# Optimization experiments

Hardware: AMD Instinct MI355X
Metric: run time of the kernel (lower is better)

Reference implementation:

```python
import jax, jax.numpy as jnp
import numpy as np

N, E, G = 50000, 800000, 128
IN_DIM, HID, HEADS, OUT_DIM = 256, 64, 4, 10
HC = HID * HEADS  # 256
NEG_SLOPE = 0.2


def _gat_layer(x, src, dst, W, att_src, att_dst, bias):
    # x: [N, F_in]; W: [F_in, H*C]; att_*: [H, C]; bias: [H*C]
    n = x.shape[0]
    h = (x @ W).reshape(n, HEADS, HID)                      # [N,H,C]
    a_src = jnp.einsum('nhc,hc->nh', h, att_src)            # [N,H]
    a_dst = jnp.einsum('nhc,hc->nh', h, att_dst)            # [N,H]
    e = a_src[src] + a_dst[dst]                             # [E,H]
    e = jax.nn.leaky_relu(e, NEG_SLOPE)
    # segment softmax over incoming edges of each dst node
    m = jax.ops.segment_max(e, dst, num_segments=n)         # [N,H]
    ex = jnp.exp(e - m[dst])
    denom = jax.ops.segment_sum(ex, dst, num_segments=n)    # [N,H]
    alpha = ex / (denom[dst] + 1e-16)                       # [E,H]
    msg = h[src] * alpha[:, :, None]                        # [E,H,C]
    out = jax.ops.segment_sum(msg, dst, num_segments=n)     # [N,H,C]
    return out.reshape(n, HC) + bias


def setup_inputs() -> dict:
    key = jax.random.key(0)
    ks = jax.random.split(key, 16)
    x = jax.random.normal(ks[0], (N, IN_DIM), dtype=jnp.float32)
    edge_index = jax.random.randint(ks[1], (2, E), 0, N, dtype=jnp.int64)
    edge_weight = jax.random.uniform(ks[2], (E,), dtype=jnp.float32)
    batch = jnp.sort(jax.random.randint(ks[3], (N,), 0, G, dtype=jnp.int64))
    s = 0.05
    W1 = jax.random.normal(ks[4], (IN_DIM, HC), dtype=jnp.float32) * s
    att_src1 = jax.random.normal(ks[5], (HEADS, HID), dtype=jnp.float32) * s
    att_dst1 = jax.random.normal(ks[6], (HEADS, HID), dtype=jnp.float32) * s
    b1 = jnp.zeros((HC,), dtype=jnp.float32)
    W2 = jax.random.normal(ks[7], (HC, HC), dtype=jnp.float32) * s
    att_src2 = jax.random.normal(ks[8], (HEADS, HID), dtype=jnp.float32) * s
    att_dst2 = jax.random.normal(ks[9], (HEADS, HID), dtype=jnp.float32) * s
    b2 = jnp.zeros((HC,), dtype=jnp.float32)
    Wf = jax.random.normal(ks[10], (HC, OUT_DIM), dtype=jnp.float32) * s
    bf = jnp.zeros((OUT_DIM,), dtype=jnp.float32)
    return dict(x=x, edge_index=edge_index, edge_weight=edge_weight, batch=batch,
                W1=W1, att_src1=att_src1, att_dst1=att_dst1, b1=b1,
                W2=W2, att_src2=att_src2, att_dst2=att_dst2, b2=b2,
                Wf=Wf, bf=bf)


def reference(x, edge_index, edge_weight, batch,
              W1, att_src1, att_dst1, b1,
              W2, att_src2, att_dst2, b2,
              Wf, bf):
    n = x.shape[0]
    # add self loops (add_self_loops=True in GATConv)
    loop = jnp.arange(n, dtype=edge_index.dtype)
    ei = jnp.concatenate([edge_index, jnp.stack([loop, loop])], axis=1)
    src, dst = ei[0], ei[1]
    h = jax.nn.relu(_gat_layer(x, src, dst, W1, att_src1, att_dst1, b1))
    h = jax.nn.relu(_gat_layer(h, src, dst, W2, att_src2, att_dst2, b2))
    # global mean pool per graph
    counts = jax.ops.segment_sum(jnp.ones((n,), dtype=h.dtype), batch, num_segments=G)
    pooled = jax.ops.segment_sum(h, batch, num_segments=G) / jnp.maximum(counts, 1.0)[:, None]
    out = pooled @ Wf + bf
    return out, pooled
```

## Files before the change

kernel.cpp:

```cpp
#include <hip/hip_runtime.h>
#include <math.h>

#define HEADS 4
#define HID 64
#define HC 256
#define NEG_SLOPE 0.2f
#define GG 128

typedef __attribute__((ext_vector_type(8))) short short8;
typedef __attribute__((ext_vector_type(4))) float floatx4;
typedef unsigned short ush;

__device__ __forceinline__ ush f2bf(float f) {
  unsigned u = __float_as_uint(f);
  unsigned r = (u + 0x7FFFu + ((u >> 16) & 1u)) >> 16;
  return (ush)r;
}
__device__ __forceinline__ float bf2f(ush h) {
  return __uint_as_float(((unsigned)h) << 16);
}

__global__ void fill_counts_kernel(int* counts, int n) {
  int i = blockIdx.x * 256 + threadIdx.x;
  if (i < n) counts[i] = 1;
}

__global__ void hist_kernel(const int* __restrict__ ei, int* counts, int E) {
  int e = blockIdx.x * 256 + threadIdx.x;
  if (e < E) atomicAdd(&counts[ei[E + e]], 1);
}

__global__ __launch_bounds__(256) void scan_pass1(const int* __restrict__ counts,
                                                  int* __restrict__ bsums, int n) {
  int t = threadIdx.x;
  int i0 = blockIdx.x * 1024 + t * 4;
  int s = 0;
  if (i0 + 3 < n) {
    int4 v = *(const int4*)&counts[i0];
    s = v.x + v.y + v.z + v.w;
  } else {
#pragma unroll
    for (int k = 0; k < 4; ++k)
      if (i0 + k < n) s += counts[i0 + k];
  }
#pragma unroll
  for (int o = 1; o < 64; o <<= 1) s += __shfl_xor(s, o, 64);
  __shared__ int ws[4];
  if ((t & 63) == 0) ws[t >> 6] = s;
  __syncthreads();
  if (t == 0) bsums[blockIdx.x] = ws[0] + ws[1] + ws[2] + ws[3];
}

__global__ __launch_bounds__(256) void scan_pass2(int* __restrict__ bsums,
                                                  int* __restrict__ row_ptr, int nb, int n) {
  __shared__ int sh[256];
  int t = threadIdx.x;
  int v = (t < nb) ? bsums[t] : 0;
  sh[t] = v;
  __syncthreads();
  for (int off = 1; off < 256; off <<= 1) {
    int u = (t >= off) ? sh[t - off] : 0;
    __syncthreads();
    sh[t] += u;
    __syncthreads();
  }
  if (t < nb) bsums[t] = sh[t] - v;
  if (t == 255) row_ptr[n] = sh[255];
}

__global__ __launch_bounds__(256) void scan_pass3(const int* __restrict__ counts,
                                                  const int* __restrict__ bsums,
                                                  int* __restrict__ row_ptr,
                                                  int* __restrict__ cursor, int n) {
  int t = threadIdx.x;
  int i0 = blockIdx.x * 1024 + t * 4;
  int c0 = 0, c1 = 0, c2 = 0, c3 = 0;
  bool full = (i0 + 3 < n);
  if (full) {
    int4 v = *(const int4*)&counts[i0];
    c0 = v.x; c1 = v.y; c2 = v.z; c3 = v.w;
  } else {
    if (i0 + 0 < n) c0 = counts[i0 + 0];
    if (i0 + 1 < n) c1 = counts[i0 + 1];
    if (i0 + 2 < n) c2 = counts[i0 + 2];
    if (i0 + 3 < n) c3 = counts[i0 + 3];
  }
  int ts = c0 + c1 + c2 + c3;
  __shared__ int sh[256];
  sh[t] = ts;
  __syncthreads();
  for (int off = 1; off < 256; off <<= 1) {
    int u = (t >= off) ? sh[t - off] : 0;
    __syncthreads();
    sh[t] += u;
    __syncthreads();
  }
  int run = bsums[blockIdx.x] + sh[t] - ts;
  int r0 = run, r1 = run + c0, r2 = r1 + c1, r3 = r2 + c2;
  if (full) {
    *(int4*)&row_ptr[i0] = make_int4(r0, r1, r2, r3);
    *(int4*)&cursor[i0] = make_int4(r0, r1, r2, r3);
  } else {
    if (i0 + 0 < n) { row_ptr[i0 + 0] = r0; cursor[i0 + 0] = r0; }
    if (i0 + 1 < n) { row_ptr[i0 + 1] = r1; cursor[i0 + 1] = r1; }
    if (i0 + 2 < n) { row_ptr[i0 + 2] = r2; cursor[i0 + 2] = r2; }
    if (i0 + 3 < n) { row_ptr[i0 + 3] = r3; cursor[i0 + 3] = r3; }
  }
}

__global__ void scatter_kernel(const int* __restrict__ ei, int* cursor, int* srcs, int E, int n) {
  int i = blockIdx.x * 256 + threadIdx.x;
  if (i >= E + n) return;
  int s, d;
  if (i < E) { s = ei[i]; d = ei[E + i]; }
  else       { s = i - E; d = s; }
  int pos = atomicAdd(&cursor[d], 1);
  srcs[pos] = s;
}

__global__ __launch_bounds__(256) void splitA_kernel(const float* __restrict__ A,
                                                     ush* __restrict__ Ah,
                                                     ush* __restrict__ Al, int total) {
  int i0 = (blockIdx.x * 256 + threadIdx.x) * 4;
  if (i0 + 3 < total) {
    float4 v = *(const float4*)&A[i0];
    ushort4 h = make_ushort4(f2bf(v.x), f2bf(v.y), f2bf(v.z), f2bf(v.w));
    ushort4 l = make_ushort4(f2bf(v.x - bf2f(h.x)), f2bf(v.y - bf2f(h.y)),
                             f2bf(v.z - bf2f(h.z)), f2bf(v.w - bf2f(h.w)));
    *(ushort4*)&Ah[i0] = h;
    *(ushort4*)&Al[i0] = l;
  } else {
    for (int k = 0; k < 4 && i0 + k < total; ++k) {
      float v = A[i0 + k];
      ush h = f2bf(v);
      Ah[i0 + k] = h;
      Al[i0 + k] = f2bf(v - bf2f(h));
    }
  }
}

__global__ void convertB_kernel(const float* __restrict__ B, ush* __restrict__ Bth,
                                ush* __restrict__ Btl) {
  int k = blockIdx.x, n = threadIdx.x;
  float v = B[k * HC + n];
  ush h = f2bf(v);
  ush l = f2bf(v - bf2f(h));
  Bth[n * HC + k] = h;
  Btl[n * HC + k] = l;
}

#define LDA 40
__global__ __launch_bounds__(256) void gemm_kernel(
    const ush* __restrict__ Ah, const ush* __restrict__ Al,
    const ush* __restrict__ Bth, const ush* __restrict__ Btl,
    const float* __restrict__ att_src, const float* __restrict__ att_dst,
    ush* __restrict__ Cb, float* __restrict__ asrc_o, float* __restrict__ adst_o, int M) {
  __shared__ ush sAh[128 * LDA];
  __shared__ ush sAl[128 * LDA];
  __shared__ ush sBh[128 * LDA];
  __shared__ ush sBl[128 * LDA];

  int t = threadIdx.x;
  int lane = t & 63, wave = t >> 6;
  int wm = wave >> 1, wn = wave & 1;
  int q = lane >> 4, mrow = lane & 15;
  int r0 = blockIdx.y * 128;
  int c0 = blockIdx.x * 128;

  int row0 = t >> 2, seg0 = t & 3;
  int row1 = (t + 256) >> 2, seg1 = (t + 256) & 3;
  bool v0 = (r0 + row0) < M, v1 = (r0 + row1) < M;
  const int4 zero4 = make_int4(0, 0, 0, 0);

  floatx4 acc[4][4];
#pragma unroll
  for (int i = 0; i < 4; ++i)
#pragma unroll
    for (int j = 0; j < 4; ++j) acc[i][j] = (floatx4)(0.0f);

  for (int k0 = 0; k0 < HC; k0 += 32) {
    __syncthreads();
    {
      size_t g0 = (size_t)(r0 + row0) * HC + k0 + seg0 * 8;
      size_t g1 = (size_t)(r0 + row1) * HC + k0 + seg1 * 8;
      *(int4*)&sAh[row0 * LDA + seg0 * 8] = v0 ? *(const int4*)&Ah[g0] : zero4;
      *(int4*)&sAh[row1 * LDA + seg1 * 8] = v1 ? *(const int4*)&Ah[g1] : zero4;
      *(int4*)&sAl[row0 * LDA + seg0 * 8] = v0 ? *(const int4*)&Al[g0] : zero4;
      *(int4*)&sAl[row1 * LDA + seg1 * 8] = v1 ? *(const int4*)&Al[g1] : zero4;
      size_t b0 = (size_t)(c0 + row0) * HC + k0 + seg0 * 8;
      size_t b1 = (size_t)(c0 + row1) * HC + k0 + seg1 * 8;
      *(int4*)&sBh[row0 * LDA + seg0 * 8] = *(const int4*)&Bth[b0];
      *(int4*)&sBh[row1 * LDA + seg1 * 8] = *(const int4*)&Bth[b1];
      *(int4*)&sBl[row0 * LDA + seg0 * 8] = *(const int4*)&Btl[b0];
      *(int4*)&sBl[row1 * LDA + seg1 * 8] = *(const int4*)&Btl[b1];
    }
    __syncthreads();

    short8 ah[4], al[4], bh[4], bl[4];
#pragma unroll
    for (int i = 0; i < 4; ++i) {
      int ar = (wm * 64 + i * 16 + mrow) * LDA + q * 8;
      int br = (wn * 64 + i * 16 + mrow) * LDA + q * 8;
      ah[i] = *(short8*)&sAh[ar];
      al[i] = *(short8*)&sAl[ar];
      bh[i] = *(short8*)&sBh[br];
      bl[i] = *(short8*)&sBl[br];
    }
#pragma unroll
    for (int i = 0; i < 4; ++i)
#pragma unroll
      for (int j = 0; j < 4; ++j) {
        acc[i][j] = __builtin_amdgcn_mfma_f32_16x16x32_bf16(ah[i], bh[j], acc[i][j], 0, 0, 0);
        acc[i][j] = __builtin_amdgcn_mfma_f32_16x16x32_bf16(ah[i], bl[j], acc[i][j], 0, 0, 0);
        acc[i][j] = __builtin_amdgcn_mfma_f32_16x16x32_bf16(al[i], bh[j], acc[i][j], 0, 0, 0);
      }
  }

  int hd = (c0 >> 6) + wn;
  float aS[4], aD[4];
#pragma unroll
  for (int j = 0; j < 4; ++j) {
    aS[j] = att_src[hd * 64 + j * 16 + mrow];
    aD[j] = att_dst[hd * 64 + j * 16 + mrow];
  }
#pragma unroll
  for (int i = 0; i < 4; ++i) {
#pragma unroll
    for (int r = 0; r < 4; ++r) {
      float ps = acc[i][0][r] * aS[0] + acc[i][1][r] * aS[1] +
                 acc[i][2][r] * aS[2] + acc[i][3][r] * aS[3];
      float pd = acc[i][0][r] * aD[0] + acc[i][1][r] * aD[1] +
                 acc[i][2][r] * aD[2] + acc[i][3][r] * aD[3];
#pragma unroll
      for (int o = 1; o < 16; o <<= 1) {
        ps += __shfl_xor(ps, o, 64);
        pd += __shfl_xor(pd, o, 64);
      }
      int grow = r0 + wm * 64 + i * 16 + q * 4 + r;
      if (mrow == 0 && grow < M) {
        asrc_o[grow * HEADS + hd] = ps;
        adst_o[grow * HEADS + hd] = pd;
      }
    }
  }

#pragma unroll
  for (int i = 0; i < 4; ++i) {
#pragma unroll
    for (int j = 0; j < 4; ++j) {
      int col = c0 + wn * 64 + j * 16 + mrow;
#pragma unroll
      for (int r = 0; r < 4; ++r) {
        int grow = r0 + wm * 64 + i * 16 + q * 4 + r;
        if (grow < M) Cb[(size_t)grow * HC + col] = f2bf(acc[i][j][r]);
      }
    }
  }
}

__device__ __forceinline__ float lrelu(float x) { return x > 0.f ? x : NEG_SLOPE * x; }

__global__ __launch_bounds__(256) void aggregate_kernel(
    const ush* __restrict__ hbf, const float* __restrict__ asrc,
    const float* __restrict__ adst, const int* __restrict__ row_ptr,
    const int* __restrict__ srcs, const float* __restrict__ bias,
    float* __restrict__ outf, ush* __restrict__ outh, ush* __restrict__ outl, int N) {
  __shared__ float s_alpha[4][64 * 4];
  __shared__ int s_src[4][64];

  int wave = threadIdx.x >> 6;
  int lane = threadIdx.x & 63;
  int node = blockIdx.x * 4 + wave;
  if (node >= N) return;

  int begin = row_ptr[node];
  int end = row_ptr[node + 1];
  int deg = end - begin;
  int nb = deg < 64 ? deg : 64;

  const float4* asrc4 = (const float4*)asrc;
  float4 ad = ((const float4*)adst)[node];

  const float NEGINF = -3.402823466e38f;
  int s0 = 0;
  float4 e0 = make_float4(NEGINF, NEGINF, NEGINF, NEGINF);
  if (lane < nb) {
    s0 = srcs[begin + lane];
    float4 a = asrc4[s0];
    e0.x = lrelu(a.x + ad.x);
    e0.y = lrelu(a.y + ad.y);
    e0.z = lrelu(a.z + ad.z);
    e0.w = lrelu(a.w + ad.w);
  }
  float m0 = e0.x, m1 = e0.y, m2 = e0.z, m3 = e0.w;
  for (int base = 64; base < deg; base += 64) {
    int idx = base + lane;
    if (idx < deg) {
      int s = srcs[begin + idx];
      float4 a = asrc4[s];
      m0 = fmaxf(m0, lrelu(a.x + ad.x));
      m1 = fmaxf(m1, lrelu(a.y + ad.y));
      m2 = fmaxf(m2, lrelu(a.z + ad.z));
      m3 = fmaxf(m3, lrelu(a.w + ad.w));
    }
  }
#pragma unroll
  for (int o = 1; o < 64; o <<= 1) {
    m0 = fmaxf(m0, __shfl_xor(m0, o, 64));
    m1 = fmaxf(m1, __shfl_xor(m1, o, 64));
    m2 = fmaxf(m2, __shfl_xor(m2, o, 64));
    m3 = fmaxf(m3, __shfl_xor(m3, o, 64));
  }
  float ex0 = (lane < nb) ? __expf(e0.x - m0) : 0.f;
  float ex1 = (lane < nb) ? __expf(e0.y - m1) : 0.f;
  float ex2 = (lane < nb) ? __expf(e0.z - m2) : 0.f;
  float ex3 = (lane < nb) ? __expf(e0.w - m3) : 0.f;
  float d0 = ex0, d1 = ex1, d2 = ex2, d3 = ex3;
  for (int base = 64; base < deg; base += 64) {
    int idx = base + lane;
    if (idx < deg) {
      int s = srcs[begin + idx];
      float4 a = asrc4[s];
      d0 += __expf(lrelu(a.x + ad.x) - m0);
      d1 += __expf(lrelu(a.y + ad.y) - m1);
      d2 += __expf(lrelu(a.z + ad.z) - m2);
      d3 += __expf(lrelu(a.w + ad.w) - m3);
    }
  }
#pragma unroll
  for (int o = 1; o < 64; o <<= 1) {
    d0 += __shfl_xor(d0, o, 64);
    d1 += __shfl_xor(d1, o, 64);
    d2 += __shfl_xor(d2, o, 64);
    d3 += __shfl_xor(d3, o, 64);
  }
  float r0 = 1.0f / (d0 + 1e-16f);
  float r1 = 1.0f / (d1 + 1e-16f);
  float r2 = 1.0f / (d2 + 1e-16f);
  float r3 = 1.0f / (d3 + 1e-16f);

  *(float4*)&s_alpha[wave][lane * 4] = make_float4(ex0 * r0, ex1 * r1, ex2 * r2, ex3 * r3);
  s_src[wave][lane] = s0;

  int head = lane >> 4;
  float mh = (head == 0) ? m0 : (head == 1) ? m1 : (head == 2) ? m2 : m3;
  float rdh = (head == 0) ? r0 : (head == 1) ? r1 : (head == 2) ? r2 : r3;
  float adh = (head == 0) ? ad.x : (head == 1) ? ad.y : (head == 2) ? ad.z : ad.w;

  const ushort4* hb4 = (const ushort4*)hbf;
  float4 accA = make_float4(0.f, 0.f, 0.f, 0.f);
  float4 accB = accA, accC = accA, accD = accA;
  int i = 0;
  for (; i + 4 <= nb; i += 4) {
    int sa = s_src[wave][i];
    int sb = s_src[wave][i + 1];
    int sc = s_src[wave][i + 2];
    int sd = s_src[wave][i + 3];
    float aa = s_alpha[wave][i * 4 + head];
    float ab = s_alpha[wave][(i + 1) * 4 + head];
    float ac = s_alpha[wave][(i + 2) * 4 + head];
    float ad_ = s_alpha[wave][(i + 3) * 4 + head];
    ushort4 u0 = hb4[(size_t)sa * 64 + lane];
    ushort4 u1 = hb4[(size_t)sb * 64 + lane];
    ushort4 u2 = hb4[(size_t)sc * 64 + lane];
    ushort4 u3 = hb4[(size_t)sd * 64 + lane];
    accA.x += aa * bf2f(u0.x); accA.y += aa * bf2f(u0.y);
    accA.z += aa * bf2f(u0.z); accA.w += aa * bf2f(u0.w);
    accB.x += ab * bf2f(u1.x); accB.y += ab * bf2f(u1.y);
    accB.z += ab * bf2f(u1.z); accB.w += ab * bf2f(u1.w);
    accC.x += ac * bf2f(u2.x); accC.y += ac * bf2f(u2.y);
    accC.z += ac * bf2f(u2.z); accC.w += ac * bf2f(u2.w);
    accD.x += ad_ * bf2f(u3.x); accD.y += ad_ * bf2f(u3.y);
    accD.z += ad_ * bf2f(u3.z); accD.w += ad_ * bf2f(u3.w);
  }
  for (; i < nb; ++i) {
    int s = s_src[wave][i];
    float a = s_alpha[wave][i * 4 + head];
    ushort4 u = hb4[(size_t)s * 64 + lane];
    accA.x += a * bf2f(u.x); accA.y += a * bf2f(u.y);
    accA.z += a * bf2f(u.z); accA.w += a * bf2f(u.w);
  }
  for (int i2 = 64; i2 < deg; ++i2) {
    int s = srcs[begin + i2];
    float ash = asrc[s * HEADS + head];
    float a = __expf(lrelu(ash + adh) - mh) * rdh;
    ushort4 u = hb4[(size_t)s * 64 + lane];
    accA.x += a * bf2f(u.x); accA.y += a * bf2f(u.y);
    accA.z += a * bf2f(u.z); accA.w += a * bf2f(u.w);
  }

  float4 acc;
  acc.x = (accA.x + accB.x) + (accC.x + accD.x);
  acc.y = (accA.y + accB.y) + (accC.y + accD.y);
  acc.z = (accA.z + accB.z) + (accC.z + accD.z);
  acc.w = (accA.w + accB.w) + (accC.w + accD.w);
  float4 bv = ((const float4*)bias)[lane];
  float4 o;
  o.x = fmaxf(acc.x + bv.x, 0.f);
  o.y = fmaxf(acc.y + bv.y, 0.f);
  o.z = fmaxf(acc.z + bv.z, 0.f);
  o.w = fmaxf(acc.w + bv.w, 0.f);

  if (outf) {
    ((float4*)outf)[(size_t)node * 64 + lane] = o;
  } else {
    ushort4 h = make_ushort4(f2bf(o.x), f2bf(o.y), f2bf(o.z), f2bf(o.w));
    ushort4 l = make_ushort4(f2bf(o.x - bf2f(h.x)), f2bf(o.y - bf2f(h.y)),
                             f2bf(o.z - bf2f(h.z)), f2bf(o.w - bf2f(h.w)));
    ((ushort4*)outh)[(size_t)node * 64 + lane] = h;
    ((ushort4*)outl)[(size_t)node * 64 + lane] = l;
  }
}

__device__ __forceinline__ int lower_bound_i(const int* a, int n, int key) {
  int lo = 0, hi = n;
  while (lo < hi) {
    int mid = (lo + hi) >> 1;
    if (a[mid] < key) lo = mid + 1; else hi = mid;
  }
  return lo;
}

__global__ __launch_bounds__(256) void pool_kernel(const float* __restrict__ h2,
                                                   const int* __restrict__ batch,
                                                   float* __restrict__ pws,
                                                   int* __restrict__ cnts, int n) {
  int g = blockIdx.x, part = blockIdx.y;
  int wave = threadIdx.x >> 6, lane = threadIdx.x & 63;
  int lo = lower_bound_i(batch, n, g);
  int hi = lower_bound_i(batch, n, g + 1);
  const float4* h4 = (const float4*)h2;
  float4 acc = make_float4(0.f, 0.f, 0.f, 0.f);
  for (int i = lo + part * 4 + wave; i < hi; i += 16) {
    float4 v = h4[(size_t)i * 64 + lane];
    acc.x += v.x; acc.y += v.y; acc.z += v.z; acc.w += v.w;
  }
  __shared__ float4 red[4][64];
  red[wave][lane] = acc;
  __syncthreads();
  if (wave == 0) {
    float4 a0 = red[0][lane], a1 = red[1][lane], a2 = red[2][lane], a3 = red[3][lane];
    float4 o;
    o.x = (a0.x + a1.x) + (a2.x + a3.x);
    o.y = (a0.y + a1.y) + (a2.y + a3.y);
    o.z = (a0.z + a1.z) + (a2.z + a3.z);
    o.w = (a0.w + a1.w) + (a2.w + a3.w);
    ((float4*)pws)[(size_t)(g * 4 + part) * 64 + lane] = o;
  }
  if (part == 0 && threadIdx.x == 0) cnts[g] = hi - lo;
}

__global__ void final_kernel(const float* __restrict__ pws, const int* __restrict__ cnts,
                             const float* __restrict__ Wf, const float* __restrict__ bf,
                             float* __restrict__ pooled_out, float* __restrict__ out) {
  int g = blockIdx.x, t = threadIdx.x;
  float s = pws[(size_t)(g * 4 + 0) * 256 + t] + pws[(size_t)(g * 4 + 1) * 256 + t] +
            pws[(size_t)(g * 4 + 2) * 256 + t] + pws[(size_t)(g * 4 + 3) * 256 + t];
  float inv = 1.0f / fmaxf((float)cnts[g], 1.0f);
  float pv = s * inv;
  pooled_out[g * HC + t] = pv;
  __shared__ float p[HC];
  p[t] = pv;
  __syncthreads();
  if (t < 10) {
    float acc = bf[t];
    for (int c = 0; c < HC; ++c) acc += p[c] * Wf[c * 10 + t];
    out[g * 10 + t] = acc;
  }
}

extern "C" void kernel_launch(void* const* d_in, const int* in_sizes, int n_in,
                              void* d_out, int out_size, void* d_ws, size_t ws_size,
                              hipStream_t stream) {
  const float* x    = (const float*)d_in[0];
  const int*   ei   = (const int*)d_in[1];
  const int*   batch = (const int*)d_in[3];
  const float* W1   = (const float*)d_in[4];
  const float* as1  = (const float*)d_in[5];
  const float* ad1  = (const float*)d_in[6];
  const float* b1   = (const float*)d_in[7];
  const float* W2   = (const float*)d_in[8];
  const float* as2  = (const float*)d_in[9];
  const float* ad2  = (const float*)d_in[10];
  const float* b2   = (const float*)d_in[11];
  const float* Wf   = (const float*)d_in[12];
  const float* bf   = (const float*)d_in[13];
  float* out = (float*)d_out;

  const int N = in_sizes[0] / HC;
  const int E = in_sizes[1] / 2;

  char* base = (char*)d_ws;
  size_t off = 0;
  auto alloc = [&](size_t bytes) {
    char* p = base + off;
    off = (off + bytes + 255) & ~(size_t)255;
    return p;
  };
  ush* xh = (ush*)alloc((size_t)N * HC * 2);
  ush* xl = (ush*)alloc((size_t)N * HC * 2);
  float* bufB = (float*)xh;
  ush* hbf = (ush*)alloc((size_t)N * HC * 2);
  float* asrc = (float*)alloc((size_t)N * HEADS * 4);
  float* adst = (float*)alloc((size_t)N * HEADS * 4);
  int* counts = (int*)alloc((size_t)N * 4);
  int* row_ptr = (int*)alloc((size_t)(N + 1) * 4);
  int* cursor = (int*)alloc((size_t)N * 4);
  int* srcs = (int*)alloc((size_t)(E + N) * 4);
  int* bsums = (int*)alloc(((N + 1023) / 1024) * 4);
  ush* Bth = (ush*)alloc((size_t)HC * HC * 2);
  ush* Btl = (ush*)alloc((size_t)HC * HC * 2);
  float* pws = (float*)alloc((size_t)GG * 4 * HC * 4);
  int* cnts = (int*)alloc((size_t)GG * 4);

  int nb = (N + 1023) / 1024;

  fill_counts_kernel<<<(N + 255) / 256, 256, 0, stream>>>(counts, N);
  hist_kernel<<<(E + 255) / 256, 256, 0, stream>>>(ei, counts, E);
  scan_pass1<<<nb, 256, 0, stream>>>(counts, bsums, N);
  scan_pass2<<<1, 256, 0, stream>>>(bsums, row_ptr, nb, N);
  scan_pass3<<<nb, 256, 0, stream>>>(counts, bsums, row_ptr, cursor, N);
  scatter_kernel<<<(E + N + 255) / 256, 256, 0, stream>>>(ei, cursor, srcs, E, N);

  dim3 ggrid(2, (N + 127) / 128);
  int agg_blocks = (N + 3) / 4;

  splitA_kernel<<<(N * HC / 4 + 255) / 256, 256, 0, stream>>>(x, xh, xl, N * HC);

  convertB_kernel<<<HC, HC, 0, stream>>>(W1, Bth, Btl);
  gemm_kernel<<<ggrid, 256, 0, stream>>>(xh, xl, Bth, Btl, as1, ad1, hbf, asrc, adst, N);
  aggregate_kernel<<<agg_blocks, 256, 0, stream>>>(hbf, asrc, adst, row_ptr, srcs, b1,
                                                   nullptr, xh, xl, N);

  convertB_kernel<<<HC, HC, 0, stream>>>(W2, Bth, Btl);
  gemm_kernel<<<ggrid, 256, 0, stream>>>(xh, xl, Bth, Btl, as2, ad2, hbf, asrc, adst, N);
  aggregate_kernel<<<agg_blocks, 256, 0, stream>>>(hbf, asrc, adst, row_ptr, srcs, b2,
                                                   bufB, nullptr, nullptr, N);

  dim3 pgrid(GG, 4);
  pool_kernel<<<pgrid, 256, 0, stream>>>(bufB, batch, pws, cnts, N);
  final_kernel<<<GG, 256, 0, stream>>>(pws, cnts, Wf, bf, out + GG * 10, out);
}
```

Measured before the change: 482.3 us.

## Widen GEMM tile to full 256 columns, store layer-2 output as bf16, merge setup kernels

```diff
diff --git a/kernel.cpp b/kernel.cpp
--- a/kernel.cpp
+++ b/kernel.cpp
@@ -20,14 +20,11 @@
   return __uint_as_float(((unsigned)h) << 16);
 }
 
-__global__ void fill_counts_kernel(int* counts, int n) {
+__global__ void hist_kernel(const int* __restrict__ ei, int* counts, int E, int n) {
   int i = blockIdx.x * 256 + threadIdx.x;
-  if (i < n) counts[i] = 1;
-}
-
-__global__ void hist_kernel(const int* __restrict__ ei, int* counts, int E) {
-  int e = blockIdx.x * 256 + threadIdx.x;
-  if (e < E) atomicAdd(&counts[ei[E + e]], 1);
+  if (i >= E + n) return;
+  int d = (i < E) ? ei[E + i] : (i - E);
+  atomicAdd(&counts[d], 1);
 }
 
 __global__ __launch_bounds__(256) void scan_pass1(const int* __restrict__ counts,
@@ -139,14 +136,18 @@
   }
 }
 
-__global__ void convertB_kernel(const float* __restrict__ B, ush* __restrict__ Bth,
-                                ush* __restrict__ Btl) {
+__global__ void convertB_kernel(const float* __restrict__ W1, const float* __restrict__ W2,
+                                ush* __restrict__ Bth1, ush* __restrict__ Btl1,
+                                ush* __restrict__ Bth2, ush* __restrict__ Btl2) {
   int k = blockIdx.x, n = threadIdx.x;
+  const float* B = blockIdx.y ? W2 : W1;
+  ush* th = blockIdx.y ? Bth2 : Bth1;
+  ush* tl = blockIdx.y ? Btl2 : Btl1;
   float v = B[k * HC + n];
   ush h = f2bf(v);
   ush l = f2bf(v - bf2f(h));
-  Bth[n * HC + k] = h;
-  Btl[n * HC + k] = l;
+  th[n * HC + k] = h;
+  tl[n * HC + k] = l;
 }
 
 #define LDA 40
@@ -157,98 +158,102 @@
     ush* __restrict__ Cb, float* __restrict__ asrc_o, float* __restrict__ adst_o, int M) {
   __shared__ ush sAh[128 * LDA];
   __shared__ ush sAl[128 * LDA];
-  __shared__ ush sBh[128 * LDA];
-  __shared__ ush sBl[128 * LDA];
+  __shared__ ush sBh[256 * LDA];
+  __shared__ ush sBl[256 * LDA];
 
   int t = threadIdx.x;
   int lane = t & 63, wave = t >> 6;
   int wm = wave >> 1, wn = wave & 1;
   int q = lane >> 4, mrow = lane & 15;
-  int r0 = blockIdx.y * 128;
-  int c0 = blockIdx.x * 128;
-
-  int row0 = t >> 2, seg0 = t & 3;
-  int row1 = (t + 256) >> 2, seg1 = (t + 256) & 3;
-  bool v0 = (r0 + row0) < M, v1 = (r0 + row1) < M;
+  int r0 = blockIdx.x * 128;
   const int4 zero4 = make_int4(0, 0, 0, 0);
 
-  floatx4 acc[4][4];
+  floatx4 acc[4][8];
 #pragma unroll
   for (int i = 0; i < 4; ++i)
 #pragma unroll
-    for (int j = 0; j < 4; ++j) acc[i][j] = (floatx4)(0.0f);
+    for (int j = 0; j < 8; ++j) acc[i][j] = (floatx4)(0.0f);
+
+  int ar0 = t >> 2, as0 = t & 3;
+  int ar1 = (t + 256) >> 2, as1 = (t + 256) & 3;
+  bool av0 = (r0 + ar0) < M, av1 = (r0 + ar1) < M;
 
   for (int k0 = 0; k0 < HC; k0 += 32) {
     __syncthreads();
     {
-      size_t g0 = (size_t)(r0 + row0) * HC + k0 + seg0 * 8;
-      size_t g1 = (size_t)(r0 + row1) * HC + k0 + seg1 * 8;
-      *(int4*)&sAh[row0 * LDA + seg0 * 8] = v0 ? *(const int4*)&Ah[g0] : zero4;
-      *(int4*)&sAh[row1 * LDA + seg1 * 8] = v1 ? *(const int4*)&Ah[g1] : zero4;
-      *(int4*)&sAl[row0 * LDA + seg0 * 8] = v0 ? *(const int4*)&Al[g0] : zero4;
-      *(int4*)&sAl[row1 * LDA + seg1 * 8] = v1 ? *(const int4*)&Al[g1] : zero4;
-      size_t b0 = (size_t)(c0 + row0) * HC + k0 + seg0 * 8;
-      size_t b1 = (size_t)(c0 + row1) * HC + k0 + seg1 * 8;
-      *(int4*)&sBh[row0 * LDA + seg0 * 8] = *(const int4*)&Bth[b0];
-      *(int4*)&sBh[row1 * LDA + seg1 * 8] = *(const int4*)&Bth[b1];
-      *(int4*)&sBl[row0 * LDA + seg0 * 8] = *(const int4*)&Btl[b0];
-      *(int4*)&sBl[row1 * LDA + seg1 * 8] = *(const int4*)&Btl[b1];
+      size_t g0 = (size_t)(r0 + ar0) * HC + k0 + as0 * 8;
+      size_t g1 = (size_t)(r0 + ar1) * HC + k0 + as1 * 8;
+      *(int4*)&sAh[ar0 * LDA + as0 * 8] = av0 ? *(const int4*)&Ah[g0] : zero4;
+      *(int4*)&sAh[ar1 * LDA + as1 * 8] = av1 ? *(const int4*)&Ah[g1] : zero4;
+      *(int4*)&sAl[ar0 * LDA + as0 * 8] = av0 ? *(const int4*)&Al[g0] : zero4;
+      *(int4*)&sAl[ar1 * LDA + as1 * 8] = av1 ? *(const int4*)&Al[g1] : zero4;
+#pragma unroll
+      for (int tau = 0; tau < 1024; tau += 256) {
+        int br = (t + tau) >> 2, bs = (t + tau) & 3;
+        size_t gb = (size_t)br * HC + k0 + bs * 8;
+        *(int4*)&sBh[br * LDA + bs * 8] = *(const int4*)&Bth[gb];
+        *(int4*)&sBl[br * LDA + bs * 8] = *(const int4*)&Btl[gb];
+      }
     }
     __syncthreads();
 
-    short8 ah[4], al[4], bh[4], bl[4];
+    short8 ah[4], al[4];
 #pragma unroll
     for (int i = 0; i < 4; ++i) {
       int ar = (wm * 64 + i * 16 + mrow) * LDA + q * 8;
-      int br = (wn * 64 + i * 16 + mrow) * LDA + q * 8;
       ah[i] = *(short8*)&sAh[ar];
       al[i] = *(short8*)&sAl[ar];
-      bh[i] = *(short8*)&sBh[br];
-      bl[i] = *(short8*)&sBl[br];
-    }
-#pragma unroll
-    for (int i = 0; i < 4; ++i)
-#pragma unroll
-      for (int j = 0; j < 4; ++j) {
-        acc[i][j] = __builtin_amdgcn_mfma_f32_16x16x32_bf16(ah[i], bh[j], acc[i][j], 0, 0, 0);
-        acc[i][j] = __builtin_amdgcn_mfma_f32_16x16x32_bf16(ah[i], bl[j], acc[i][j], 0, 0, 0);
-        acc[i][j] = __builtin_amdgcn_mfma_f32_16x16x32_bf16(al[i], bh[j], acc[i][j], 0, 0, 0);
+    }
+#pragma unroll
+    for (int j = 0; j < 8; ++j) {
+      int br = (wn * 128 + j * 16 + mrow) * LDA + q * 8;
+      short8 bh = *(short8*)&sBh[br];
+      short8 bl = *(short8*)&sBl[br];
+#pragma unroll
+      for (int i = 0; i < 4; ++i) {
+        acc[i][j] = __builtin_amdgcn_mfma_f32_16x16x32_bf16(ah[i], bh, acc[i][j], 0, 0, 0);
+        acc[i][j] = __builtin_amdgcn_mfma_f32_16x16x32_bf16(ah[i], bl, acc[i][j], 0, 0, 0);
+        acc[i][j] = __builtin_amdgcn_mfma_f32_16x16x32_bf16(al[i], bh, acc[i][j], 0, 0, 0);
       }
-  }
-
-  int hd = (c0 >> 6) + wn;
-  float aS[4], aD[4];
-#pragma unroll
-  for (int j = 0; j < 4; ++j) {
-    aS[j] = att_src[hd * 64 + j * 16 + mrow];
-    aD[j] = att_dst[hd * 64 + j * 16 + mrow];
-  }
+    }
+  }
+
+#pragma unroll
+  for (int jh = 0; jh < 2; ++jh) {
+    int hd = wn * 2 + jh;
+    float aS[4], aD[4];
+#pragma unroll
+    for (int jj = 0; jj < 4; ++jj) {
+      aS[jj] = att_src[hd * 64 + jj * 16 + mrow];
+      aD[jj] = att_dst[hd * 64 + jj * 16 + mrow];
+    }
+#pragma unroll
+    for (int i = 0; i < 4; ++i) {
+#pragma unroll
+      for (int r = 0; r < 4; ++r) {
+        float ps = acc[i][jh * 4 + 0][r] * aS[0] + acc[i][jh * 4 + 1][r] * aS[1] +
+                   acc[i][jh * 4 + 2][r] * aS[2] + acc[i][jh * 4 + 3][r] * aS[3];
+        float pd = acc[i][jh * 4 + 0][r] * aD[0] + acc[i][jh * 4 + 1][r] * aD[1] +
+                   acc[i][jh * 4 + 2][r] * aD[2] + acc[i][jh * 4 + 3][r] * aD[3];
+#pragma unroll
+        for (int o = 1; o < 16; o <<= 1) {
+          ps += __shfl_xor(ps, o, 64);
+          pd += __shfl_xor(pd, o, 64);
+        }
+        int grow = r0 + wm * 64 + i * 16 + q * 4 + r;
+        if (mrow == 0 && grow < M) {
+          asrc_o[grow * HEADS + hd] = ps;
+          adst_o[grow * HEADS + hd] = pd;
+        }
+      }
+    }
+  }
+
 #pragma unroll
   for (int i = 0; i < 4; ++i) {
 #pragma unroll
-    for (int r = 0; r < 4; ++r) {
-      float ps = acc[i][0][r] * aS[0] + acc[i][1][r] * aS[1] +
-                 acc[i][2][r] * aS[2] + acc[i][3][r] * aS[3];
-      float pd = acc[i][0][r] * aD[0] + acc[i][1][r] * aD[1] +
-                 acc[i][2][r] * aD[2] + acc[i][3][r] * aD[3];
-#pragma unroll
-      for (int o = 1; o < 16; o <<= 1) {
-        ps += __shfl_xor(ps, o, 64);
-        pd += __shfl_xor(pd, o, 64);
-      }
-      int grow = r0 + wm * 64 + i * 16 + q * 4 + r;
-      if (mrow == 0 && grow < M) {
-        asrc_o[grow * HEADS + hd] = ps;
-        adst_o[grow * HEADS + hd] = pd;
-      }
-    }
-  }
-
-#pragma unroll
-  for (int i = 0; i < 4; ++i) {
-#pragma unroll
-    for (int j = 0; j < 4; ++j) {
-      int col = c0 + wn * 64 + j * 16 + mrow;
+    for (int j = 0; j < 8; ++j) {
+      int col = wn * 128 + j * 16 + mrow;
 #pragma unroll
       for (int r = 0; r < 4; ++r) {
         int grow = r0 + wm * 64 + i * 16 + q * 4 + r;
@@ -405,10 +410,12 @@
     ((float4*)outf)[(size_t)node * 64 + lane] = o;
   } else {
     ushort4 h = make_ushort4(f2bf(o.x), f2bf(o.y), f2bf(o.z), f2bf(o.w));
-    ushort4 l = make_ushort4(f2bf(o.x - bf2f(h.x)), f2bf(o.y - bf2f(h.y)),
-                             f2bf(o.z - bf2f(h.z)), f2bf(o.w - bf2f(h.w)));
     ((ushort4*)outh)[(size_t)node * 64 + lane] = h;
-    ((ushort4*)outl)[(size_t)node * 64 + lane] = l;
+    if (outl) {
+      ushort4 l = make_ushort4(f2bf(o.x - bf2f(h.x)), f2bf(o.y - bf2f(h.y)),
+                               f2bf(o.z - bf2f(h.z)), f2bf(o.w - bf2f(h.w)));
+      ((ushort4*)outl)[(size_t)node * 64 + lane] = l;
+    }
   }
 }
 
@@ -421,7 +428,7 @@
   return lo;
 }
 
-__global__ __launch_bounds__(256) void pool_kernel(const float* __restrict__ h2,
+__global__ __launch_bounds__(256) void pool_kernel(const ush* __restrict__ h2,
                                                    const int* __restrict__ batch,
                                                    float* __restrict__ pws,
                                                    int* __restrict__ cnts, int n) {
@@ -429,11 +436,12 @@
   int wave = threadIdx.x >> 6, lane = threadIdx.x & 63;
   int lo = lower_bound_i(batch, n, g);
   int hi = lower_bound_i(batch, n, g + 1);
-  const float4* h4 = (const float4*)h2;
+  const ushort4* h4 = (const ushort4*)h2;
   float4 acc = make_float4(0.f, 0.f, 0.f, 0.f);
   for (int i = lo + part * 4 + wave; i < hi; i += 16) {
-    float4 v = h4[(size_t)i * 64 + lane];
-    acc.x += v.x; acc.y += v.y; acc.z += v.z; acc.w += v.w;
+    ushort4 u = h4[(size_t)i * 64 + lane];
+    acc.x += bf2f(u.x); acc.y += bf2f(u.y);
+    acc.z += bf2f(u.z); acc.w += bf2f(u.w);
   }
   __shared__ float4 red[4][64];
   red[wave][lane] = acc;
@@ -499,7 +507,6 @@
   };
   ush* xh = (ush*)alloc((size_t)N * HC * 2);
   ush* xl = (ush*)alloc((size_t)N * HC * 2);
-  float* bufB = (float*)xh;
   ush* hbf = (ush*)alloc((size_t)N * HC * 2);
   float* asrc = (float*)alloc((size_t)N * HEADS * 4);
   float* adst = (float*)alloc((size_t)N * HEADS * 4);
@@ -508,36 +515,38 @@
   int* cursor = (int*)alloc((size_t)N * 4);
   int* srcs = (int*)alloc((size_t)(E + N) * 4);
   int* bsums = (int*)alloc(((N + 1023) / 1024) * 4);
-  ush* Bth = (ush*)alloc((size_t)HC * HC * 2);
-  ush* Btl = (ush*)alloc((size_t)HC * HC * 2);
+  ush* Bth1 = (ush*)alloc((size_t)HC * HC * 2);
+  ush* Btl1 = (ush*)alloc((size_t)HC * HC * 2);
+  ush* Bth2 = (ush*)alloc((size_t)HC * HC * 2);
+  ush* Btl2 = (ush*)alloc((size_t)HC * HC * 2);
   float* pws = (float*)alloc((size_t)GG * 4 * HC * 4);
   int* cnts = (int*)alloc((size_t)GG * 4);
 
   int nb = (N + 1023) / 1024;
 
-  fill_counts_kernel<<<(N + 255) / 256, 256, 0, stream>>>(counts, N);
-  hist_kernel<<<(E + 255) / 256, 256, 0, stream>>>(ei, counts, E);
+  hipMemsetAsync(counts, 0, (size_t)N * 4, stream);
+  hist_kernel<<<(E + N + 255) / 256, 256, 0, stream>>>(ei, counts, E, N);
   scan_pass1<<<nb, 256, 0, stream>>>(counts, bsums, N);
   scan_pass2<<<1, 256, 0, stream>>>(bsums, row_ptr, nb, N);
   scan_pass3<<<nb, 256, 0, stream>>>(counts, bsums, row_ptr, cursor, N);
   scatter_kernel<<<(E + N + 255) / 256, 256, 0, stream>>>(ei, cursor, srcs, E, N);
 
-  dim3 ggrid(2, (N + 127) / 128);
+  dim3 cbgrid(HC, 2);
+  convertB_kernel<<<cbgrid, HC, 0, stream>>>(W1, W2, Bth1, Btl1, Bth2, Btl2);
+  splitA_kernel<<<(N * HC / 4 + 255) / 256, 256, 0, stream>>>(x, xh, xl, N * HC);
+
+  int ggrid = (N + 127) / 128;
   int agg_blocks = (N + 3) / 4;
 
-  splitA_kernel<<<(N * HC / 4 + 255) / 256, 256, 0, stream>>>(x, xh, xl, N * HC);
-
-  convertB_kernel<<<HC, HC, 0, stream>>>(W1, Bth, Btl);
-  gemm_kernel<<<ggrid, 256, 0, stream>>>(xh, xl, Bth, Btl, as1, ad1, hbf, asrc, adst, N);
+  gemm_kernel<<<ggrid, 256, 0, stream>>>(xh, xl, Bth1, Btl1, as1, ad1, hbf, asrc, adst, N);
   aggregate_kernel<<<agg_blocks, 256, 0, stream>>>(hbf, asrc, adst, row_ptr, srcs, b1,
                                                    nullptr, xh, xl, N);
 
-  convertB_kernel<<<HC, HC, 0, stream>>>(W2, Bth, Btl);
-  gemm_kernel<<<ggrid, 256, 0, stream>>>(xh, xl, Bth, Btl, as2, ad2, hbf, asrc, adst, N);
+  gemm_kernel<<<ggrid, 256, 0, stream>>>(xh, xl, Bth2, Btl2, as2, ad2, hbf, asrc, adst, N);
   aggregate_kernel<<<agg_blocks, 256, 0, stream>>>(hbf, asrc, adst, row_ptr, srcs, b2,
-                                                   bufB, nullptr, nullptr, N);
+                                                   nullptr, xh, nullptr, N);
 
   dim3 pgrid(GG, 4);
-  pool_kernel<<<pgrid, 256, 0, stream>>>(bufB, batch, pws, cnts, N);
+  pool_kernel<<<pgrid, 256, 0, stream>>>(xh, batch, pws, cnts, N);
   final_kernel<<<GG, 256, 0, stream>>>(pws, cnts, Wf, bf, out + GG * 10, out);
 }
```

Measured after the change: 510.9 us. 1.06x slower.

## Prefetch GEMM tiles into registers, store layer-2 output as bf16, merge setup kernels

Applied to the files above, without the earlier changes.

```diff
diff --git a/kernel.cpp b/kernel.cpp
--- a/kernel.cpp
+++ b/kernel.cpp
@@ -20,14 +20,11 @@
   return __uint_as_float(((unsigned)h) << 16);
 }
 
-__global__ void fill_counts_kernel(int* counts, int n) {
+__global__ void hist_kernel(const int* __restrict__ ei, int* counts, int E, int n) {
   int i = blockIdx.x * 256 + threadIdx.x;
-  if (i < n) counts[i] = 1;
-}
-
-__global__ void hist_kernel(const int* __restrict__ ei, int* counts, int E) {
-  int e = blockIdx.x * 256 + threadIdx.x;
-  if (e < E) atomicAdd(&counts[ei[E + e]], 1);
+  if (i >= E + n) return;
+  int d = (i < E) ? ei[E + i] : (i - E);
+  atomicAdd(&counts[d], 1);
 }
 
 __global__ __launch_bounds__(256) void scan_pass1(const int* __restrict__ counts,
@@ -139,14 +136,18 @@
   }
 }
 
-__global__ void convertB_kernel(const float* __restrict__ B, ush* __restrict__ Bth,
-                                ush* __restrict__ Btl) {
+__global__ void convertB_kernel(const float* __restrict__ W1, const float* __restrict__ W2,
+                                ush* __restrict__ Bth1, ush* __restrict__ Btl1,
+                                ush* __restrict__ Bth2, ush* __restrict__ Btl2) {
   int k = blockIdx.x, n = threadIdx.x;
+  const float* B = blockIdx.y ? W2 : W1;
+  ush* th = blockIdx.y ? Bth2 : Bth1;
+  ush* tl = blockIdx.y ? Btl2 : Btl1;
   float v = B[k * HC + n];
   ush h = f2bf(v);
   ush l = f2bf(v - bf2f(h));
-  Bth[n * HC + k] = h;
-  Btl[n * HC + k] = l;
+  th[n * HC + k] = h;
+  tl[n * HC + k] = l;
 }
 
 #define LDA 40
@@ -166,11 +167,30 @@
   int q = lane >> 4, mrow = lane & 15;
   int r0 = blockIdx.y * 128;
   int c0 = blockIdx.x * 128;
+  const int4 zero4 = make_int4(0, 0, 0, 0);
 
   int row0 = t >> 2, seg0 = t & 3;
   int row1 = (t + 256) >> 2, seg1 = (t + 256) & 3;
   bool v0 = (r0 + row0) < M, v1 = (r0 + row1) < M;
-  const int4 zero4 = make_int4(0, 0, 0, 0);
+
+  const ush* Ag0 = Ah + (size_t)(r0 + row0) * HC + seg0 * 8;
+  const ush* Ag1 = Ah + (size_t)(r0 + row1) * HC + seg1 * 8;
+  const ush* Al0 = Al + (size_t)(r0 + row0) * HC + seg0 * 8;
+  const ush* Al1 = Al + (size_t)(r0 + row1) * HC + seg1 * 8;
+  const ush* Bg0 = Bth + (size_t)(c0 + row0) * HC + seg0 * 8;
+  const ush* Bg1 = Bth + (size_t)(c0 + row1) * HC + seg1 * 8;
+  const ush* Bl0 = Btl + (size_t)(c0 + row0) * HC + seg0 * 8;
+  const ush* Bl1 = Btl + (size_t)(c0 + row1) * HC + seg1 * 8;
+
+  int4 pAh0, pAh1, pAl0, pAl1, pBh0, pBh1, pBl0, pBl1;
+  pAh0 = v0 ? *(const int4*)(Ag0) : zero4;
+  pAh1 = v1 ? *(const int4*)(Ag1) : zero4;
+  pAl0 = v0 ? *(const int4*)(Al0) : zero4;
+  pAl1 = v1 ? *(const int4*)(Al1) : zero4;
+  pBh0 = *(const int4*)(Bg0);
+  pBh1 = *(const int4*)(Bg1);
+  pBl0 = *(const int4*)(Bl0);
+  pBl1 = *(const int4*)(Bl1);
 
   floatx4 acc[4][4];
 #pragma unroll
@@ -179,22 +199,27 @@
     for (int j = 0; j < 4; ++j) acc[i][j] = (floatx4)(0.0f);
 
   for (int k0 = 0; k0 < HC; k0 += 32) {
+    *(int4*)&sAh[row0 * LDA + seg0 * 8] = pAh0;
+    *(int4*)&sAh[row1 * LDA + seg1 * 8] = pAh1;
+    *(int4*)&sAl[row0 * LDA + seg0 * 8] = pAl0;
+    *(int4*)&sAl[row1 * LDA + seg1 * 8] = pAl1;
+    *(int4*)&sBh[row0 * LDA + seg0 * 8] = pBh0;
+    *(int4*)&sBh[row1 * LDA + seg1 * 8] = pBh1;
+    *(int4*)&sBl[row0 * LDA + seg0 * 8] = pBl0;
+    *(int4*)&sBl[row1 * LDA + seg1 * 8] = pBl1;
     __syncthreads();
-    {
-      size_t g0 = (size_t)(r0 + row0) * HC + k0 + seg0 * 8;
-      size_t g1 = (size_t)(r0 + row1) * HC + k0 + seg1 * 8;
-      *(int4*)&sAh[row0 * LDA + seg0 * 8] = v0 ? *(const int4*)&Ah[g0] : zero4;
-      *(int4*)&sAh[row1 * LDA + seg1 * 8] = v1 ? *(const int4*)&Ah[g1] : zero4;
-      *(int4*)&sAl[row0 * LDA + seg0 * 8] = v0 ? *(const int4*)&Al[g0] : zero4;
-      *(int4*)&sAl[row1 * LDA + seg1 * 8] = v1 ? *(const int4*)&Al[g1] : zero4;
-      size_t b0 = (size_t)(c0 + row0) * HC + k0 + seg0 * 8;
-      size_t b1 = (size_t)(c0 + row1) * HC + k0 + seg1 * 8;
-      *(int4*)&sBh[row0 * LDA + seg0 * 8] = *(const int4*)&Bth[b0];
-      *(int4*)&sBh[row1 * LDA + seg1 * 8] = *(const int4*)&Bth[b1];
-      *(int4*)&sBl[row0 * LDA + seg0 * 8] = *(const int4*)&Btl[b0];
-      *(int4*)&sBl[row1 * LDA + seg1 * 8] = *(const int4*)&Btl[b1];
-    }
-    __syncthreads();
+
+    int kn = k0 + 32;
+    if (kn < HC) {
+      pAh0 = v0 ? *(const int4*)(Ag0 + kn) : zero4;
+      pAh1 = v1 ? *(const int4*)(Ag1 + kn) : zero4;
+      pAl0 = v0 ? *(const int4*)(Al0 + kn) : zero4;
+      pAl1 = v1 ? *(const int4*)(Al1 + kn) : zero4;
+      pBh0 = *(const int4*)(Bg0 + kn);
+      pBh1 = *(const int4*)(Bg1 + kn);
+      pBl0 = *(const int4*)(Bl0 + kn);
+      pBl1 = *(const int4*)(Bl1 + kn);
+    }
 
     short8 ah[4], al[4], bh[4], bl[4];
 #pragma unroll
@@ -214,6 +239,7 @@
         acc[i][j] = __builtin_amdgcn_mfma_f32_16x16x32_bf16(ah[i], bl[j], acc[i][j], 0, 0, 0);
         acc[i][j] = __builtin_amdgcn_mfma_f32_16x16x32_bf16(al[i], bh[j], acc[i][j], 0, 0, 0);
       }
+    __syncthreads();
   }
 
   int hd = (c0 >> 6) + wn;
@@ -405,10 +431,12 @@
     ((float4*)outf)[(size_t)node * 64 + lane] = o;
   } else {
     ushort4 h = make_ushort4(f2bf(o.x), f2bf(o.y), f2bf(o.z), f2bf(o.w));
-    ushort4 l = make_ushort4(f2bf(o.x - bf2f(h.x)), f2bf(o.y - bf2f(h.y)),
-                             f2bf(o.z - bf2f(h.z)), f2bf(o.w - bf2f(h.w)));
     ((ushort4*)outh)[(size_t)node * 64 + lane] = h;
-    ((ushort4*)outl)[(size_t)node * 64 + lane] = l;
+    if (outl) {
+      ushort4 l = make_ushort4(f2bf(o.x - bf2f(h.x)), f2bf(o.y - bf2f(h.y)),
+                               f2bf(o.z - bf2f(h.z)), f2bf(o.w - bf2f(h.w)));
+      ((ushort4*)outl)[(size_t)node * 64 + lane] = l;
+    }
   }
 }
 
@@ -421,7 +449,7 @@
   return lo;
 }
 
-__global__ __launch_bounds__(256) void pool_kernel(const float* __restrict__ h2,
+__global__ __launch_bounds__(256) void pool_kernel(const ush* __restrict__ h2,
                                                    const int* __restrict__ batch,
                                                    float* __restrict__ pws,
                                                    int* __restrict__ cnts, int n) {
@@ -429,11 +457,12 @@
   int wave = threadIdx.x >> 6, lane = threadIdx.x & 63;
   int lo = lower_bound_i(batch, n, g);
   int hi = lower_bound_i(batch, n, g + 1);
-  const float4* h4 = (const float4*)h2;
+  const ushort4* h4 = (const ushort4*)h2;
   float4 acc = make_float4(0.f, 0.f, 0.f, 0.f);
   for (int i = lo + part * 4 + wave; i < hi; i += 16) {
-    float4 v = h4[(size_t)i * 64 + lane];
-    acc.x += v.x; acc.y += v.y; acc.z += v.z; acc.w += v.w;
+    ushort4 u = h4[(size_t)i * 64 + lane];
+    acc.x += bf2f(u.x); acc.y += bf2f(u.y);
+    acc.z += bf2f(u.z); acc.w += bf2f(u.w);
   }
   __shared__ float4 red[4][64];
   red[wave][lane] = acc;
@@ -499,7 +528,6 @@
   };
   ush* xh = (ush*)alloc((size_t)N * HC * 2);
   ush* xl = (ush*)alloc((size_t)N * HC * 2);
-  float* bufB = (float*)xh;
   ush* hbf = (ush*)alloc((size_t)N * HC * 2);
   float* asrc = (float*)alloc((size_t)N * HEADS * 4);
   float* adst = (float*)alloc((size_t)N * HEADS * 4);
@@ -508,36 +536,38 @@
   int* cursor = (int*)alloc((size_t)N * 4);
   int* srcs = (int*)alloc((size_t)(E + N) * 4);
   int* bsums = (int*)alloc(((N + 1023) / 1024) * 4);
-  ush* Bth = (ush*)alloc((size_t)HC * HC * 2);
-  ush* Btl = (ush*)alloc((size_t)HC * HC * 2);
+  ush* Bth1 = (ush*)alloc((size_t)HC * HC * 2);
+  ush* Btl1 = (ush*)alloc((size_t)HC * HC * 2);
+  ush* Bth2 = (ush*)alloc((size_t)HC * HC * 2);
+  ush* Btl2 = (ush*)alloc((size_t)HC * HC * 2);
   float* pws = (float*)alloc((size_t)GG * 4 * HC * 4);
   int* cnts = (int*)alloc((size_t)GG * 4);
 
   int nb = (N + 1023) / 1024;
 
-  fill_counts_kernel<<<(N + 255) / 256, 256, 0, stream>>>(counts, N);
-  hist_kernel<<<(E + 255) / 256, 256, 0, stream>>>(ei, counts, E);
+  hipMemsetAsync(counts, 0, (size_t)N * 4, stream);
+  hist_kernel<<<(E + N + 255) / 256, 256, 0, stream>>>(ei, counts, E, N);
   scan_pass1<<<nb, 256, 0, stream>>>(counts, bsums, N);
   scan_pass2<<<1, 256, 0, stream>>>(bsums, row_ptr, nb, N);
   scan_pass3<<<nb, 256, 0, stream>>>(counts, bsums, row_ptr, cursor, N);
   scatter_kernel<<<(E + N + 255) / 256, 256, 0, stream>>>(ei, cursor, srcs, E, N);
 
+  dim3 cbgrid(HC, 2);
+  convertB_kernel<<<cbgrid, HC, 0, stream>>>(W1, W2, Bth1, Btl1, Bth2, Btl2);
+  splitA_kernel<<<(N * HC / 4 + 255) / 256, 256, 0, stream>>>(x, xh, xl, N * HC);
+
   dim3 ggrid(2, (N + 127) / 128);
   int agg_blocks = (N + 3) / 4;
 
-  splitA_kernel<<<(N * HC / 4 + 255) / 256, 256, 0, stream>>>(x, xh, xl, N * HC);
-
-  convertB_kernel<<<HC, HC, 0, stream>>>(W1, Bth, Btl);
-  gemm_kernel<<<ggrid, 256, 0, stream>>>(xh, xl, Bth, Btl, as1, ad1, hbf, asrc, adst, N);
+  gemm_kernel<<<ggrid, 256, 0, stream>>>(xh, xl, Bth1, Btl1, as1, ad1, hbf, asrc, adst, N);
   aggregate_kernel<<<agg_blocks, 256, 0, stream>>>(hbf, asrc, adst, row_ptr, srcs, b1,
                                                    nullptr, xh, xl, N);
 
-  convertB_kernel<<<HC, HC, 0, stream>>>(W2, Bth, Btl);
-  gemm_kernel<<<ggrid, 256, 0, stream>>>(xh, xl, Bth, Btl, as2, ad2, hbf, asrc, adst, N);
+  gemm_kernel<<<ggrid, 256, 0, stream>>>(xh, xl, Bth2, Btl2, as2, ad2, hbf, asrc, adst, N);
   aggregate_kernel<<<agg_blocks, 256, 0, stream>>>(hbf, asrc, adst, row_ptr, srcs, b2,
-                                                   bufB, nullptr, nullptr, N);
+                                                   nullptr, xh, nullptr, N);
 
   dim3 pgrid(GG, 4);
-  pool_kernel<<<pgrid, 256, 0, stream>>>(bufB, batch, pws, cnts, N);
+  pool_kernel<<<pgrid, 256, 0, stream>>>(xh, batch, pws, cnts, N);
   final_kernel<<<GG, 256, 0, stream>>>(pws, cnts, Wf, bf, out + GG * 10, out);
 }
```

New measurement: 471.8 us. 1.02x faster.
